# Performance work log

Measured on AMD Instinct MI355X. Metric: run time of the kernel, lower is better.

Reference implementation:

```python
import jax, jax.numpy as jnp
import numpy as np

D_MODEL = 1024
D_FF = 4096
N_EXPERTS = 8
TOP_K = 2
B, S = 4, 2048


def setup_inputs() -> dict:
    key = jax.random.key(0)
    ks = jax.random.split(key, 6)
    x = jax.random.normal(ks[0], (B, S, D_MODEL), dtype=jnp.float32)
    # router gate: nn.Linear(d_model, num_experts, bias=False), weight [E, D]
    gate_w = jax.random.normal(ks[1], (N_EXPERTS, D_MODEL), dtype=jnp.float32) * 0.01
    # expert MLPs, xavier-uniform init
    lim1 = float(np.sqrt(6.0 / (D_MODEL + D_FF)))
    W1 = jax.random.uniform(ks[2], (N_EXPERTS, D_FF, D_MODEL), minval=-lim1, maxval=lim1, dtype=jnp.float32)
    b1 = jnp.zeros((N_EXPERTS, D_FF), dtype=jnp.float32)
    W2 = jax.random.uniform(ks[3], (N_EXPERTS, D_MODEL, D_FF), minval=-lim1, maxval=lim1, dtype=jnp.float32)
    b2 = jnp.zeros((N_EXPERTS, D_MODEL), dtype=jnp.float32)
    return {"x": x, "gate_w": gate_w, "W1": W1, "b1": b1, "W2": W2, "b2": b2}


def reference(x, gate_w, W1, b1, W2, b2):
    Bb, Ss, D = x.shape
    xt = x.reshape(-1, D)                                  # [N, D]
    # --- router ---
    logits = xt @ gate_w.T                                 # [N, E]
    probs = jax.nn.softmax(logits, axis=-1)
    w_topk, idx = jax.lax.top_k(probs, TOP_K)              # [N, K]
    w_topk = w_topk / (jnp.sum(w_topk, axis=-1, keepdims=True) + 1e-9)
    # dense combine weights: zero for unselected experts    [N, E]
    comb = jnp.sum(jax.nn.one_hot(idx, N_EXPERTS, dtype=xt.dtype) * w_topk[..., None], axis=1)
    # --- experts (dense grouped GEMM over all experts) ---
    h = jnp.einsum('nd,efd->enf', xt, W1) + b1[:, None, :]  # [E, N, ff]
    h = jax.nn.relu(h)                                      # dropout=identity (eval)
    y = jnp.einsum('enf,edf->end', h, W2) + b2[:, None, :]  # [E, N, D]
    # --- weighted scatter/combine ---
    out = jnp.einsum('ne,end->nd', comb, y)                 # [N, D]
    return out.reshape(Bb, Ss, D)
```

## Files before the change

kernel.cpp:

```cpp
#include <hip/hip_runtime.h>
#include <hip/hip_bf16.h>
#include <stdint.h>

#define D_MODEL 1024
#define D_FF    4096
#define N_EXP   8
#define TOPK    2
#define NTOK    8192
#define NASSIGN (NTOK*TOPK)

#define BM 128
#define BN 128
#define BK 64
#define THREADS 256

typedef __bf16 bf16_t;
typedef __attribute__((ext_vector_type(8))) bf16_t bf16x8;
typedef __attribute__((ext_vector_type(4))) float f32x4;

__device__ __forceinline__ unsigned short f2bf(float f) {
    bf16_t b = (bf16_t)f;
    return __builtin_bit_cast(unsigned short, b);
}

__device__ __forceinline__ void gload_lds16(const void* g, void* l) {
    __builtin_amdgcn_global_load_lds(
        (const __attribute__((address_space(1))) void*)g,
        (__attribute__((address_space(3))) void*)l, 16, 0, 0);
}

__global__ void zero_out_kernel(float* __restrict__ out, int n, int* __restrict__ counts) {
    if (blockIdx.x == 0 && threadIdx.x < N_EXP) counts[threadIdx.x] = 0;
    int stride = gridDim.x * blockDim.x;
    float4 z = make_float4(0.f, 0.f, 0.f, 0.f);
    for (int i = blockIdx.x * blockDim.x + threadIdx.x; i < n / 4; i += stride)
        ((float4*)out)[i] = z;
}

__global__ void cvt_bf16_kernel(const float* __restrict__ in, unsigned short* __restrict__ outp, int n) {
    int stride = gridDim.x * blockDim.x;
    for (int i = blockIdx.x * blockDim.x + threadIdx.x; i < n / 4; i += stride) {
        float4 v = ((const float4*)in)[i];
        ushort4 o;
        o.x = f2bf(v.x); o.y = f2bf(v.y); o.z = f2bf(v.z); o.w = f2bf(v.w);
        ((ushort4*)outp)[i] = o;
    }
}

__global__ __launch_bounds__(64) void router_kernel(
        const float* __restrict__ x, const float* __restrict__ gw,
        int* __restrict__ counts, int* __restrict__ ltok, float* __restrict__ lw) {
    int n = blockIdx.x;
    int lane = threadIdx.x;
    const float* xr = x + (size_t)n * D_MODEL;
    float acc[N_EXP];
    #pragma unroll
    for (int e = 0; e < N_EXP; e++) acc[e] = 0.f;
    for (int d = lane; d < D_MODEL; d += 64) {
        float xv = xr[d];
        #pragma unroll
        for (int e = 0; e < N_EXP; e++) acc[e] += xv * gw[e * D_MODEL + d];
    }
    #pragma unroll
    for (int e = 0; e < N_EXP; e++) {
        #pragma unroll
        for (int off = 32; off > 0; off >>= 1)
            acc[e] += __shfl_down(acc[e], off);
    }
    if (lane == 0) {
        float mx = acc[0];
        #pragma unroll
        for (int e = 1; e < N_EXP; e++) mx = fmaxf(mx, acc[e]);
        float p[N_EXP];
        float s = 0.f;
        #pragma unroll
        for (int e = 0; e < N_EXP; e++) { p[e] = expf(acc[e] - mx); s += p[e]; }
        float inv = 1.f / s;
        #pragma unroll
        for (int e = 0; e < N_EXP; e++) p[e] *= inv;
        int i0 = 0;
        #pragma unroll
        for (int e = 1; e < N_EXP; e++) if (p[e] > p[i0]) i0 = e;
        int i1 = (i0 == 0) ? 1 : 0;
        #pragma unroll
        for (int e = 0; e < N_EXP; e++) if (e != i0 && p[e] > p[i1]) i1 = e;
        float s2 = p[i0] + p[i1] + 1e-9f;
        float w0 = p[i0] / s2, w1 = p[i1] / s2;
        int pos0 = atomicAdd(&counts[i0], 1);
        ltok[i0 * NTOK + pos0] = n; lw[i0 * NTOK + pos0] = w0;
        int pos1 = atomicAdd(&counts[i1], 1);
        ltok[i1 * NTOK + pos1] = n; lw[i1 * NTOK + pos1] = w1;
    }
}

__global__ void scan_kernel(const int* __restrict__ counts, int* __restrict__ offs) {
    if (threadIdx.x == 0 && blockIdx.x == 0) {
        int s = 0;
        for (int e = 0; e < N_EXP; e++) { offs[e] = s; s += counts[e]; }
    }
}


__global__ __launch_bounds__(THREADS, 3) void gemm1_kernel(
        const unsigned short* __restrict__ xb, const unsigned short* __restrict__ w1b,
        const float* __restrict__ b1,
        const int* __restrict__ counts, const int* __restrict__ offs,
        const int* __restrict__ ltok,
        unsigned short* __restrict__ hb) {
    const int NTM = NTOK / BM;
    int b = blockIdx.x;
    int e = b & 7;
    int idx = b >> 3;
    int nt = idx / NTM;
    int mt = idx % NTM;
    int cnt = counts[e];
    if (mt * BM >= cnt) return;

    __shared__ __align__(16) unsigned short As[BM * BK];
    __shared__ __align__(16) unsigned short Bs[BN * BK];

    int t = threadIdx.x;
    int lane = t & 63, w = t >> 6;
    int wr = w >> 1, wc = w & 1;

    int srow = t >> 3;
    int schunk = (t & 7) ^ (srow & 7);
    const unsigned short* aptr[4];
    const unsigned short* bptr[4];
    #pragma unroll
    for (int j = 0; j < 4; j++) {
        int rr = srow + j * 32;
        int slot = mt * BM + rr;
        int cs = slot < cnt ? slot : (cnt - 1);
        int tok = ltok[e * NTOK + cs];
        aptr[j] = xb + (size_t)tok * D_MODEL + schunk * 8;
        bptr[j] = w1b + ((size_t)e * D_FF + nt * BN + rr) * D_MODEL + schunk * 8;
    }
    char* As_b = (char*)As;
    char* Bs_b = (char*)Bs;

    int arow_base = wr * 64 + (lane & 15);
    int brow_base = wc * 64 + (lane & 15);
    int ch[2];
    #pragma unroll
    for (int ks = 0; ks < 2; ks++)
        ch[ks] = ((ks * 4 + (lane >> 4)) ^ (lane & 7)) << 4;

    f32x4 acc[4][4];
    #pragma unroll
    for (int m = 0; m < 4; m++)
        #pragma unroll
        for (int n = 0; n < 4; n++)
            acc[m][n] = (f32x4){0.f, 0.f, 0.f, 0.f};

    for (int k0 = 0; k0 < D_MODEL; k0 += BK) {
        #pragma unroll
        for (int j = 0; j < 4; j++) {
            gload_lds16(aptr[j] + k0, As_b + j * 4096 + t * 16);
            gload_lds16(bptr[j] + k0, Bs_b + j * 4096 + t * 16);
        }
        __syncthreads();
        bf16x8 af[2][4], bf[2][4];
        #pragma unroll
        for (int ks = 0; ks < 2; ks++) {
            #pragma unroll
            for (int m = 0; m < 4; m++)
                af[ks][m] = *(const bf16x8*)(As_b + (size_t)(arow_base + m * 16) * 128 + ch[ks]);
            #pragma unroll
            for (int n = 0; n < 4; n++)
                bf[ks][n] = *(const bf16x8*)(Bs_b + (size_t)(brow_base + n * 16) * 128 + ch[ks]);
        }
        #pragma unroll
        for (int ks = 0; ks < 2; ks++)
            #pragma unroll
            for (int m = 0; m < 4; m++)
                #pragma unroll
                for (int n = 0; n < 4; n++)
                    acc[m][n] = __builtin_amdgcn_mfma_f32_16x16x32_bf16(af[ks][m], bf[ks][n], acc[m][n], 0, 0, 0);
        __syncthreads();
    }

    int hbase = offs[e];
    float biasv[4];
    #pragma unroll
    for (int n = 0; n < 4; ++n)
        biasv[n] = b1[e * D_FF + nt * BN + wc * 64 + n * 16 + (lane & 15)];
    #pragma unroll
    for (int m = 0; m < 4; ++m) {
        int s0 = mt * BM + wr * 64 + m * 16 + (lane >> 4) * 4;
        #pragma unroll
        for (int rq = 0; rq < 4; ++rq) {
            int s = s0 + rq;
            if (s < cnt) {
                size_t rowoff = (size_t)(hbase + s) * D_FF + nt * BN + wc * 64 + (lane & 15);
                #pragma unroll
                for (int n = 0; n < 4; ++n) {
                    float v = fmaxf(acc[m][n][rq] + biasv[n], 0.f);
                    hb[rowoff + n * 16] = f2bf(v);
                }
            }
        }
    }
}

__global__ __launch_bounds__(THREADS, 3) void gemm2_kernel(
        const unsigned short* __restrict__ hb, const unsigned short* __restrict__ w2b,
        const float* __restrict__ b2,
        const int* __restrict__ counts, const int* __restrict__ offs,
        const int* __restrict__ ltok, const float* __restrict__ lw,
        float* __restrict__ out) {
    const int NTM = NTOK / BM;
    int b = blockIdx.x;
    int e = b & 7;
    int idx = b >> 3;
    int nt = idx / NTM;
    int mt = idx % NTM;
    int cnt = counts[e];
    if (mt * BM >= cnt) return;
    int hbase = offs[e];

    __shared__ __align__(16) unsigned short As[BM * BK];
    __shared__ __align__(16) unsigned short Bs[BN * BK];

    int t = threadIdx.x;
    int lane = t & 63, w = t >> 6;
    int wr = w >> 1, wc = w & 1;

    int srow = t >> 3;
    int schunk = (t & 7) ^ (srow & 7);
    const unsigned short* aptr[4];
    const unsigned short* bptr[4];
    #pragma unroll
    for (int j = 0; j < 4; j++) {
        int rr = srow + j * 32;
        int slot = mt * BM + rr;
        int cs = slot < cnt ? slot : (cnt - 1);
        aptr[j] = hb + (size_t)(hbase + cs) * D_FF + schunk * 8;
        bptr[j] = w2b + ((size_t)e * D_MODEL + nt * BN + rr) * D_FF + schunk * 8;
    }
    char* As_b = (char*)As;
    char* Bs_b = (char*)Bs;

    int arow_base = wr * 64 + (lane & 15);
    int brow_base = wc * 64 + (lane & 15);
    int ch[2];
    #pragma unroll
    for (int ks = 0; ks < 2; ks++)
        ch[ks] = ((ks * 4 + (lane >> 4)) ^ (lane & 7)) << 4;

    f32x4 acc[4][4];
    #pragma unroll
    for (int m = 0; m < 4; m++)
        #pragma unroll
        for (int n = 0; n < 4; n++)
            acc[m][n] = (f32x4){0.f, 0.f, 0.f, 0.f};

    for (int k0 = 0; k0 < D_FF; k0 += BK) {
        #pragma unroll
        for (int j = 0; j < 4; j++) {
            gload_lds16(aptr[j] + k0, As_b + j * 4096 + t * 16);
            gload_lds16(bptr[j] + k0, Bs_b + j * 4096 + t * 16);
        }
        __syncthreads();
        bf16x8 af[2][4], bf[2][4];
        #pragma unroll
        for (int ks = 0; ks < 2; ks++) {
            #pragma unroll
            for (int m = 0; m < 4; m++)
                af[ks][m] = *(const bf16x8*)(As_b + (size_t)(arow_base + m * 16) * 128 + ch[ks]);
            #pragma unroll
            for (int n = 0; n < 4; n++)
                bf[ks][n] = *(const bf16x8*)(Bs_b + (size_t)(brow_base + n * 16) * 128 + ch[ks]);
        }
        #pragma unroll
        for (int ks = 0; ks < 2; ks++)
            #pragma unroll
            for (int m = 0; m < 4; m++)
                #pragma unroll
                for (int n = 0; n < 4; n++)
                    acc[m][n] = __builtin_amdgcn_mfma_f32_16x16x32_bf16(af[ks][m], bf[ks][n], acc[m][n], 0, 0, 0);
        __syncthreads();
    }

    int lbase = e * NTOK;
    float biasv[4];
    #pragma unroll
    for (int n = 0; n < 4; ++n)
        biasv[n] = b2[e * D_MODEL + nt * BN + wc * 64 + n * 16 + (lane & 15)];
    #pragma unroll
    for (int m = 0; m < 4; ++m) {
        int s0 = mt * BM + wr * 64 + m * 16 + (lane >> 4) * 4;
        #pragma unroll
        for (int rq = 0; rq < 4; ++rq) {
            int s = s0 + rq;
            if (s >= cnt) continue;
            int tok = ltok[lbase + s];
            float wgt = lw[lbase + s];
            float* orow = out + (size_t)tok * D_MODEL + nt * BN + wc * 64 + (lane & 15);
            #pragma unroll
            for (int n = 0; n < 4; ++n)
                atomicAdd(orow + n * 16, wgt * (acc[m][n][rq] + biasv[n]));
        }
    }
}

extern "C" void kernel_launch(void* const* d_in, const int* in_sizes, int n_in,
                              void* d_out, int out_size, void* d_ws, size_t ws_size,
                              hipStream_t stream) {
    const float* x  = (const float*)d_in[0];
    const float* gw = (const float*)d_in[1];
    const float* W1 = (const float*)d_in[2];
    const float* b1 = (const float*)d_in[3];
    const float* W2 = (const float*)d_in[4];
    const float* b2 = (const float*)d_in[5];
    float* out = (float*)d_out;

    char* ws = (char*)d_ws;
    size_t off = 0;
    auto alloc = [&](size_t bytes) -> char* {
        char* p = ws + off;
        off += (bytes + 255) & ~(size_t)255;
        return p;
    };
    unsigned short* xb  = (unsigned short*)alloc((size_t)NTOK * D_MODEL * 2);
    unsigned short* w1b = (unsigned short*)alloc((size_t)N_EXP * D_FF * D_MODEL * 2);
    unsigned short* w2b = (unsigned short*)alloc((size_t)N_EXP * D_MODEL * D_FF * 2);
    unsigned short* hb  = (unsigned short*)alloc((size_t)NASSIGN * D_FF * 2);
    int*   counts = (int*)alloc(256);
    int*   offs   = (int*)alloc(256);
    int*   ltok   = (int*)alloc((size_t)N_EXP * NTOK * 4);
    float* lw     = (float*)alloc((size_t)N_EXP * NTOK * 4);

    zero_out_kernel<<<2048, 256, 0, stream>>>(out, out_size, counts);
    cvt_bf16_kernel<<<2048, 256, 0, stream>>>(x, xb, NTOK * D_MODEL);
    cvt_bf16_kernel<<<4096, 256, 0, stream>>>(W1, w1b, N_EXP * D_FF * D_MODEL);
    cvt_bf16_kernel<<<4096, 256, 0, stream>>>(W2, w2b, N_EXP * D_MODEL * D_FF);
    router_kernel<<<NTOK, 64, 0, stream>>>(x, gw, counts, ltok, lw);
    scan_kernel<<<1, 64, 0, stream>>>(counts, offs);
    gemm1_kernel<<<N_EXP * (NTOK / BM) * (D_FF / BN), THREADS, 0, stream>>>(
        xb, w1b, b1, counts, offs, ltok, hb);
    gemm2_kernel<<<N_EXP * (NTOK / BM) * (D_MODEL / BN), THREADS, 0, stream>>>(
        hb, w2b, b2, counts, offs, ltok, lw, out);
}
```

Before: 699.6 us.

## Split-K gemm2, fuse x bf16 conversion into router, raise occupancy bound

Gemm2 is split along the D_FF reduction into four chunks, so each block computes a partial sum and adds it atomically into the output, with the bias added only by the first chunk. This multiplies the number of active blocks, since only about a quarter of the per-expert M tiles actually run. The router now vectorizes its loads and writes the bf16 copy of x, which removes a separate conversion pass over x. Launch bounds for both GEMMs go from 3 to 4 waves per SIMD, which may limit registers and cause spills, and split-K quadruples the atomic traffic on the output.

```diff
diff --git a/kernel.cpp b/kernel.cpp
--- a/kernel.cpp
+++ b/kernel.cpp
@@ -13,6 +13,7 @@
 #define BN 128
 #define BK 64
 #define THREADS 256
+#define SPLITK 4
 
 typedef __bf16 bf16_t;
 typedef __attribute__((ext_vector_type(8))) bf16_t bf16x8;
@@ -49,17 +50,28 @@
 
 __global__ __launch_bounds__(64) void router_kernel(
         const float* __restrict__ x, const float* __restrict__ gw,
-        int* __restrict__ counts, int* __restrict__ ltok, float* __restrict__ lw) {
+        int* __restrict__ counts, int* __restrict__ ltok, float* __restrict__ lw,
+        unsigned short* __restrict__ xb) {
     int n = blockIdx.x;
     int lane = threadIdx.x;
     const float* xr = x + (size_t)n * D_MODEL;
+    unsigned short* xbr = xb + (size_t)n * D_MODEL;
     float acc[N_EXP];
     #pragma unroll
     for (int e = 0; e < N_EXP; e++) acc[e] = 0.f;
-    for (int d = lane; d < D_MODEL; d += 64) {
-        float xv = xr[d];
-        #pragma unroll
-        for (int e = 0; e < N_EXP; e++) acc[e] += xv * gw[e * D_MODEL + d];
+    #pragma unroll
+    for (int i = 0; i < 4; i++) {
+        int j = lane + i * 64;
+        float4 v = ((const float4*)xr)[j];
+        ushort4 o;
+        o.x = f2bf(v.x); o.y = f2bf(v.y); o.z = f2bf(v.z); o.w = f2bf(v.w);
+        ((ushort4*)xbr)[j] = o;
+        int d = j * 4;
+        #pragma unroll
+        for (int e = 0; e < N_EXP; e++) {
+            const float* g = gw + e * D_MODEL + d;
+            acc[e] += v.x * g[0] + v.y * g[1] + v.z * g[2] + v.w * g[3];
+        }
     }
     #pragma unroll
     for (int e = 0; e < N_EXP; e++) {
@@ -101,7 +113,7 @@
 }
 
 
-__global__ __launch_bounds__(THREADS, 3) void gemm1_kernel(
+__global__ __launch_bounds__(THREADS, 4) void gemm1_kernel(
         const unsigned short* __restrict__ xb, const unsigned short* __restrict__ w1b,
         const float* __restrict__ b1,
         const int* __restrict__ counts, const int* __restrict__ offs,
@@ -203,21 +215,26 @@
     }
 }
 
-__global__ __launch_bounds__(THREADS, 3) void gemm2_kernel(
+__global__ __launch_bounds__(THREADS, 4) void gemm2_kernel(
         const unsigned short* __restrict__ hb, const unsigned short* __restrict__ w2b,
         const float* __restrict__ b2,
         const int* __restrict__ counts, const int* __restrict__ offs,
         const int* __restrict__ ltok, const float* __restrict__ lw,
         float* __restrict__ out) {
     const int NTM = NTOK / BM;
+    const int NTN = D_MODEL / BN;
+    const int KC = D_FF / SPLITK;
     int b = blockIdx.x;
     int e = b & 7;
     int idx = b >> 3;
-    int nt = idx / NTM;
     int mt = idx % NTM;
+    int rest = idx / NTM;
+    int nt = rest % NTN;
+    int sk = rest / NTN;
     int cnt = counts[e];
     if (mt * BM >= cnt) return;
     int hbase = offs[e];
+    int kbase = sk * KC;
 
     __shared__ __align__(16) unsigned short As[BM * BK];
     __shared__ __align__(16) unsigned short Bs[BN * BK];
@@ -235,8 +252,8 @@
         int rr = srow + j * 32;
         int slot = mt * BM + rr;
         int cs = slot < cnt ? slot : (cnt - 1);
-        aptr[j] = hb + (size_t)(hbase + cs) * D_FF + schunk * 8;
-        bptr[j] = w2b + ((size_t)e * D_MODEL + nt * BN + rr) * D_FF + schunk * 8;
+        aptr[j] = hb + (size_t)(hbase + cs) * D_FF + kbase + schunk * 8;
+        bptr[j] = w2b + ((size_t)e * D_MODEL + nt * BN + rr) * D_FF + kbase + schunk * 8;
     }
     char* As_b = (char*)As;
     char* Bs_b = (char*)Bs;
@@ -255,7 +272,7 @@
         for (int n = 0; n < 4; n++)
             acc[m][n] = (f32x4){0.f, 0.f, 0.f, 0.f};
 
-    for (int k0 = 0; k0 < D_FF; k0 += BK) {
+    for (int k0 = 0; k0 < KC; k0 += BK) {
         #pragma unroll
         for (int j = 0; j < 4; j++) {
             gload_lds16(aptr[j] + k0, As_b + j * 4096 + t * 16);
@@ -286,7 +303,7 @@
     float biasv[4];
     #pragma unroll
     for (int n = 0; n < 4; ++n)
-        biasv[n] = b2[e * D_MODEL + nt * BN + wc * 64 + n * 16 + (lane & 15)];
+        biasv[n] = (sk == 0) ? b2[e * D_MODEL + nt * BN + wc * 64 + n * 16 + (lane & 15)] : 0.f;
     #pragma unroll
     for (int m = 0; m < 4; ++m) {
         int s0 = mt * BM + wr * 64 + m * 16 + (lane >> 4) * 4;
@@ -332,13 +349,12 @@
     float* lw     = (float*)alloc((size_t)N_EXP * NTOK * 4);
 
     zero_out_kernel<<<2048, 256, 0, stream>>>(out, out_size, counts);
-    cvt_bf16_kernel<<<2048, 256, 0, stream>>>(x, xb, NTOK * D_MODEL);
     cvt_bf16_kernel<<<4096, 256, 0, stream>>>(W1, w1b, N_EXP * D_FF * D_MODEL);
     cvt_bf16_kernel<<<4096, 256, 0, stream>>>(W2, w2b, N_EXP * D_MODEL * D_FF);
-    router_kernel<<<NTOK, 64, 0, stream>>>(x, gw, counts, ltok, lw);
+    router_kernel<<<NTOK, 64, 0, stream>>>(x, gw, counts, ltok, lw, xb);
     scan_kernel<<<1, 64, 0, stream>>>(counts, offs);
     gemm1_kernel<<<N_EXP * (NTOK / BM) * (D_FF / BN), THREADS, 0, stream>>>(
         xb, w1b, b1, counts, offs, ltok, hb);
-    gemm2_kernel<<<N_EXP * (NTOK / BM) * (D_MODEL / BN), THREADS, 0, stream>>>(
+    gemm2_kernel<<<N_EXP * (NTOK / BM) * (D_MODEL / BN) * SPLITK, THREADS, 0, stream>>>(
         hb, w2b, b2, counts, offs, ltok, lw, out);
 }
```

Result: slower. 815.7 us (+16.6%).
